# Performance work log

Hardware: AMD Instinct MI355X
Metric: run time of the kernel (lower is better)

Reference implementation:

```python
import jax, jax.numpy as jnp
import numpy as np

EPS = 1e-09


def _glorot(key, shape):
    fan_in, fan_out = shape[-2], shape[-1]
    std = (2.0 / (fan_in + fan_out)) ** 0.5
    return jax.random.normal(key, shape, dtype=jnp.float32) * std


def setup_inputs() -> dict:
    key = jax.random.key(0)
    kx, k1, k2, k3, k4 = jax.random.split(key, 5)
    B, S, D = 2, 1024, 256
    H, K = 8, 32  # key_dim_frac = 1/8
    return {
        "x": jax.random.normal(kx, (B, S, D), dtype=jnp.float32),
        "Wks": _glorot(k1, (H, D, K)),
        "Wqs": _glorot(k2, (H, D, K)),
        "Wvs": _glorot(k3, (H, D, D)),
        "Wo": _glorot(k4, (H, D, D)),
    }


def reference(x, Wks, Wqs, Wvs, Wo):
    # Per-head projections: [H, B, S, K] / [H, B, S, D]
    keys = jnp.einsum('bsd,hdk->hbsk', x, Wks)
    queries = jnp.einsum('bsd,hdk->hbsk', x, Wqs)
    values = jnp.einsum('bsd,hde->hbse', x, Wvs)

    # Feature map: elu + 1 (strictly positive)
    keys = jax.nn.elu(keys) + 1.0
    queries = jax.nn.elu(queries) + 1.0

    # Auxiliary pairwise attention map [H, B, S, S], causal-masked, row-normalized
    att = jnp.einsum('hbsk,hbtk->hbst', queries, keys)
    S = att.shape[-1]
    causal = jnp.tril(jnp.ones((S, S), dtype=att.dtype))
    att = att * causal
    att = att / (jnp.sum(att, axis=-1, keepdims=True) + EPS)

    # Causal linear attention via cumulative sums of outer products
    # [H, B, S, D, K] cumulative state (memory-bound, mirrors tf.cumsum)
    kv = jnp.einsum('hbsk,hbsd->hbsdk', keys, values)
    kv_cum = jnp.cumsum(kv, axis=2)
    numerator = jnp.einsum('hbsdk,hbsk->hbsd', kv_cum, queries)
    denominator = jnp.einsum('hbsk,hbsk->hbs', jnp.cumsum(keys, axis=2), queries)
    node = numerator / (denominator[..., None] + EPS)

    # Output projection, summed over heads: [B, S, D]
    out = jnp.einsum('hbsd,hde->bse', node, Wo)
    return (out, att)
```

## Files before the change

kernel.cpp:

```cpp
#include <hip/hip_runtime.h>
#include <hip/hip_bf16.h>
#include <cstdio>

#define PB 2
#define PS 1024
#define PD 256
#define PK 32
#define HB (PH*PB)
#define PH 8
#define BS (PB*PS)
#define EPS 1e-9f

typedef __attribute__((ext_vector_type(8))) short bf16x8;
typedef __attribute__((ext_vector_type(4))) float f32x4;

__device__ inline unsigned short f2bf(float f) {
    __hip_bfloat16 h = __float2bfloat16(f);
    return *reinterpret_cast<unsigned short*>(&h);
}

__global__ void k_xb(const float* __restrict__ x, unsigned short* __restrict__ xb) {
    int i = blockIdx.x*256 + threadIdx.x;
    float4 v = ((const float4*)x)[i];
    ushort4 o = {f2bf(v.x), f2bf(v.y), f2bf(v.z), f2bf(v.w)};
    ((ushort4*)xb)[i] = o;
}

__global__ void k_transpose_qk(const float* __restrict__ Wqs, const float* __restrict__ Wks,
                               unsigned short* __restrict__ WqT, unsigned short* __restrict__ WkT) {
    int h = blockIdx.x;
    const float* S = (blockIdx.y ? Wks : Wqs) + (size_t)h*8192;
    unsigned short* D = (blockIdx.y ? WkT : WqT) + (size_t)h*8192;
    __shared__ float T[256*33];
    int tid = threadIdx.x;
#pragma unroll
    for (int p = 0; p < 32; ++p) {
        int idx = p*256 + tid;
        T[(idx>>5)*33 + (idx&31)] = S[idx];
    }
    __syncthreads();
#pragma unroll
    for (int p = 0; p < 8; ++p) {
        int o4 = p*256 + tid;
        int kk = o4 >> 6, d = (o4 & 63)*4;
        ushort4 o;
        o.x = f2bf(T[(d+0)*33 + kk]); o.y = f2bf(T[(d+1)*33 + kk]);
        o.z = f2bf(T[(d+2)*33 + kk]); o.w = f2bf(T[(d+3)*33 + kk]);
        *(ushort4*)(D + (size_t)kk*256 + d) = o;
    }
}

__global__ void k_transpose256(const float* __restrict__ src, unsigned short* __restrict__ dst,
                               int dst_row_stride, int dst_head_stride) {
    int e0 = blockIdx.x*64, d0 = blockIdx.y*64, h = blockIdx.z;
    __shared__ float T[64][69];
    const float* S = src + (size_t)h*65536;
    int ty = threadIdx.x>>4, c4 = threadIdx.x&15;
#pragma unroll
    for (int p = 0; p < 4; ++p) {
        int r = p*16 + ty;
        float4 v = *(const float4*)(S + (size_t)(d0+r)*256 + e0 + c4*4);
        T[r][c4*4+0]=v.x; T[r][c4*4+1]=v.y; T[r][c4*4+2]=v.z; T[r][c4*4+3]=v.w;
    }
    __syncthreads();
    unsigned short* D = dst + (size_t)h*dst_head_stride;
#pragma unroll
    for (int p = 0; p < 4; ++p) {
        int er = p*16 + ty;
        ushort4 o;
        o.x = f2bf(T[c4*4+0][er]); o.y = f2bf(T[c4*4+1][er]);
        o.z = f2bf(T[c4*4+2][er]); o.w = f2bf(T[c4*4+3][er]);
        *(ushort4*)(D + (size_t)(e0+er)*dst_row_stride + d0 + c4*4) = o;
    }
}

__global__ __launch_bounds__(256) void k_proj_qk_mfma(
    const unsigned short* __restrict__ xb, const unsigned short* __restrict__ WqT,
    const unsigned short* __restrict__ WkT,
    float* __restrict__ Q, float* __restrict__ Kf,
    unsigned short* __restrict__ Qb, unsigned short* __restrict__ Kb)
{
    int m0 = blockIdx.x*64;
    int isK = blockIdx.y;
    int n0 = blockIdx.z*64;
    const unsigned short* W = isK ? WkT : WqT;
    int tid = threadIdx.x, w = tid>>6, l15 = tid&15, g = (tid>>4)&3;
    f32x4 zf = {0.f,0.f,0.f,0.f};
    f32x4 acc[4] = {zf,zf,zf,zf};
    const unsigned short* arow = xb + (size_t)(m0+16*w+l15)*256 + 8*g;
#pragma unroll
    for (int kk = 0; kk < 8; ++kk) {
        bf16x8 af = *(const bf16x8*)(arow + kk*32);
#pragma unroll
        for (int nt = 0; nt < 4; ++nt) {
            bf16x8 bf = *(const bf16x8*)(W + (size_t)(n0+16*nt+l15)*256 + kk*32 + 8*g);
            acc[nt] = __builtin_amdgcn_mfma_f32_16x16x32_bf16(af, bf, acc[nt], 0, 0, 0);
        }
    }
    int bs_base = m0 + 16*w + 4*g;
#pragma unroll
    for (int nt = 0; nt < 4; ++nt) {
        int col = n0 + 16*nt + l15;
        int h = col>>5, kk = col&31;
#pragma unroll
        for (int j = 0; j < 4; ++j) {
            int bs = bs_base + j;
            int b = bs>>10, s = bs&1023;
            float z = acc[nt][j];
            z = z > 0.f ? z + 1.f : expf(z);
            size_t idx = ((size_t)(h*PB+b)*PS + s)*PK + kk;
            if (isK) { Kf[idx] = z; Kb[idx] = f2bf(z); }
            else     { Q[idx]  = z; Qb[idx] = f2bf(z); }
        }
    }
}

__global__ void k_cumsum(const float* __restrict__ Kf, float* __restrict__ cumK) {
    int hb  = blockIdx.x;
    int tid = threadIdx.x;
    int c = tid >> 5, kk = tid & 31;
    const float* src = Kf   + hb*(PS*PK) + c*128*PK + kk;
    float*       dst = cumK + hb*(PS*PK) + c*128*PK + kk;
    float sum = 0.f;
#pragma unroll 8
    for (int i = 0; i < 128; ++i) sum += src[i*PK];
    __shared__ float ssum[8][32];
    ssum[c][kk] = sum;
    __syncthreads();
    float acc = 0.f;
    for (int j = 0; j < c; ++j) acc += ssum[j][kk];
#pragma unroll 8
    for (int i = 0; i < 128; ++i) { acc += src[i*PK]; dst[i*PK] = acc; }
}

__global__ void k_den(const float* __restrict__ Q, const float* __restrict__ cumK,
                      float* __restrict__ den) {
    int i = blockIdx.x*256 + threadIdx.x;
    const float4* q  = (const float4*)(Q    + (size_t)i*PK);
    const float4* ck = (const float4*)(cumK + (size_t)i*PK);
    float acc = 0.f;
#pragma unroll
    for (int j = 0; j < 8; ++j) {
        float4 a = q[j], b = ck[j];
        acc += a.x*b.x + a.y*b.y + a.z*b.z + a.w*b.w;
    }
    den[i] = acc + EPS;
}

__global__ __launch_bounds__(256) void k_proj_v_mfma(
    const unsigned short* __restrict__ xb, const unsigned short* __restrict__ WvT,
    unsigned short* __restrict__ Vt)
{
    int e0 = blockIdx.x*64, m0 = blockIdx.y*64, h = blockIdx.z;
    int tid = threadIdx.x, w = tid>>6, l15 = tid&15, g = (tid>>4)&3;
    f32x4 zf = {0.f,0.f,0.f,0.f};
    f32x4 acc[4] = {zf,zf,zf,zf};
    const unsigned short* arow = xb + (size_t)(m0+16*w+l15)*256 + 8*g;
    const unsigned short* Wb = WvT + (size_t)h*65536;
#pragma unroll
    for (int kk = 0; kk < 8; ++kk) {
        bf16x8 af = *(const bf16x8*)(arow + kk*32);
#pragma unroll
        for (int nt = 0; nt < 4; ++nt) {
            bf16x8 bf = *(const bf16x8*)(Wb + (size_t)(e0+16*nt+l15)*256 + kk*32 + 8*g);
            acc[nt] = __builtin_amdgcn_mfma_f32_16x16x32_bf16(af, bf, acc[nt], 0, 0, 0);
        }
    }
    unsigned short* VtT = Vt + ((size_t)h*32 + blockIdx.y)*(256*64);
#pragma unroll
    for (int nt = 0; nt < 4; ++nt) {
        ushort4 o = {f2bf(acc[nt][0]), f2bf(acc[nt][1]), f2bf(acc[nt][2]), f2bf(acc[nt][3])};
        *(ushort4*)(VtT + (size_t)(e0+16*nt+l15)*64 + 16*w + 4*g) = o;
    }
}

__global__ void k_att_zero(float* __restrict__ att) {
    int st = blockIdx.x;
    int hb = blockIdx.y;
    int s0 = st * 64;
    int c0 = s0 + 64;
    int nz4 = (PS - c0) >> 2;
    float* base = att + (size_t)hb*PS*PS + (size_t)s0*PS + c0;
    int r = threadIdx.x >> 2;
    int l4 = threadIdx.x & 3;
    float4 z = {0.f, 0.f, 0.f, 0.f};
    for (int c4 = l4; c4 < nz4; c4 += 4)
        *(float4*)(base + (size_t)r*PS + c4*4) = z;
}

__global__ __launch_bounds__(256) void k_fused(
    const unsigned short* __restrict__ Qb, const unsigned short* __restrict__ Kb,
    const float* __restrict__ den, const unsigned short* __restrict__ Vt,
    float* __restrict__ att, unsigned short* __restrict__ nodeB)
{
    int yy = blockIdx.x;
    int st = (yy & 1) ? (15 - (yy >> 1)) : (yy >> 1);
    int hb = blockIdx.y;
    int s0 = st * 64;
    int tid = threadIdx.x;
    int w = tid >> 6, l15 = tid & 15, g = (tid >> 4) & 3;

    __shared__ unsigned short VtL[256*72];
    __shared__ unsigned short PL[64*72];
    __shared__ float rden[64];

    bf16x8 qf = *(const bf16x8*)(Qb + ((size_t)hb*PS + s0 + 16*w + l15)*PK + 8*g);
    if (tid < 64) rden[tid] = 1.0f / den[hb*PS + s0 + tid];

    f32x4 zf = {0.f, 0.f, 0.f, 0.f};
    f32x4 acc2[4][4];
#pragma unroll
    for (int i = 0; i < 4; ++i)
#pragma unroll
        for (int j = 0; j < 4; ++j) acc2[i][j] = zf;

    float* attb = att + (size_t)hb*PS*PS;

    for (int t0 = 0; t0 <= s0; t0 += 64) {
        __syncthreads();
        const float4* src = (const float4*)(Vt + ((size_t)hb*16 + (t0 >> 6))*(256*64));
#pragma unroll
        for (int rep = 0; rep < 8; ++rep) {
            int idx = tid + rep*256;
            float4 v = src[idx];
            int e = idx >> 3, q = idx & 7;
            *(float4*)(VtL + e*72 + q*8) = v;
        }
        f32x4 p[4];
#pragma unroll
        for (int nt = 0; nt < 4; ++nt) {
            bf16x8 kf = *(const bf16x8*)(Kb + ((size_t)hb*PS + t0 + 16*nt + l15)*PK + 8*g);
            p[nt] = __builtin_amdgcn_mfma_f32_16x16x32_bf16(qf, kf, zf, 0, 0, 0);
        }
        bool diag = (t0 == s0);
        int rb = 16*w + 4*g;
#pragma unroll
        for (int nt = 0; nt < 4; ++nt) {
#pragma unroll
            for (int j = 0; j < 4; ++j) {
                int r = rb + j;
                int t = t0 + 16*nt + l15;
                float v = p[nt][j] * rden[r];
                if (diag && t > s0 + r) v = 0.f;
                attb[(size_t)(s0 + r)*PS + t] = v;
                PL[r*72 + 16*nt + l15] = f2bf(v);
            }
        }
        __syncthreads();
#pragma unroll
        for (int c = 0; c < 2; ++c) {
            bf16x8 af[4];
#pragma unroll
            for (int mt = 0; mt < 4; ++mt)
                af[mt] = *(const bf16x8*)(PL + (16*mt + l15)*72 + 32*c + 8*g);
#pragma unroll
            for (int ntl = 0; ntl < 4; ++ntl) {
                bf16x8 vf = *(const bf16x8*)(VtL + (16*(4*w + ntl) + l15)*72 + 32*c + 8*g);
#pragma unroll
                for (int mt = 0; mt < 4; ++mt)
                    acc2[mt][ntl] = __builtin_amdgcn_mfma_f32_16x16x32_bf16(af[mt], vf, acc2[mt][ntl], 0, 0, 0);
            }
        }
    }
    int h = hb >> 1, b = hb & 1;
    unsigned short* np = nodeB + ((size_t)(b*PS + s0))*2048 + h*256;
#pragma unroll
    for (int mt = 0; mt < 4; ++mt)
#pragma unroll
        for (int ntl = 0; ntl < 4; ++ntl)
#pragma unroll
            for (int j = 0; j < 4; ++j)
                np[(size_t)(16*mt + 4*g + j)*2048 + 64*w + 16*ntl + l15] = f2bf(acc2[mt][ntl][j]);
}

__global__ __launch_bounds__(256) void k_out_mfma(
    const unsigned short* __restrict__ nodeB, const unsigned short* __restrict__ WoT,
    float* __restrict__ part)
{
    int e0 = blockIdx.x*64, m0 = blockIdx.y*64, kz = blockIdx.z;
    int tid = threadIdx.x, w = tid>>6, l15 = tid&15, g = (tid>>4)&3;
    f32x4 zf = {0.f,0.f,0.f,0.f};
    f32x4 acc[4] = {zf,zf,zf,zf};
    const unsigned short* arow = nodeB + (size_t)(m0+16*w+l15)*2048 + kz*1024 + 8*g;
    const unsigned short* brow = WoT + kz*1024 + 8*g;
#pragma unroll
    for (int kk = 0; kk < 32; ++kk) {
        bf16x8 af = *(const bf16x8*)(arow + kk*32);
#pragma unroll
        for (int nt = 0; nt < 4; ++nt) {
            bf16x8 bf = *(const bf16x8*)(brow + (size_t)(e0+16*nt+l15)*2048 + kk*32);
            acc[nt] = __builtin_amdgcn_mfma_f32_16x16x32_bf16(af, bf, acc[nt], 0, 0, 0);
        }
    }
    float* P = part + (size_t)kz*BS*PD;
#pragma unroll
    for (int nt = 0; nt < 4; ++nt)
#pragma unroll
        for (int j = 0; j < 4; ++j)
            P[(size_t)(m0+16*w+4*g+j)*PD + e0+16*nt+l15] = acc[nt][j];
}

__global__ void k_reduce2(const float* __restrict__ part, float* __restrict__ out) {
    int i = blockIdx.x*256 + threadIdx.x;
    const float4* p = (const float4*)part;
    float4 a = p[i], b = p[131072 + i];
    float4 o = {a.x+b.x, a.y+b.y, a.z+b.z, a.w+b.w};
    ((float4*)out)[i] = o;
}

extern "C" void kernel_launch(void* const* d_in, const int* in_sizes, int n_in,
                              void* d_out, int out_size, void* d_ws, size_t ws_size,
                              hipStream_t stream) {
    const float* x   = (const float*)d_in[0];
    const float* Wks = (const float*)d_in[1];
    const float* Wqs = (const float*)d_in[2];
    const float* Wvs = (const float*)d_in[3];
    const float* Wo  = (const float*)d_in[4];

    float* out = (float*)d_out;
    float* att = (float*)d_out + (size_t)PB*PS*PD;

    float* ws = (float*)d_ws;
    float*          Q     = ws + 0;
    float*          Kf    = ws + 524288;
    float*          cumK  = ws + 1048576;
    float*          den   = ws + 1572864;
    unsigned short* Qb    = (unsigned short*)(ws + 1589248);
    unsigned short* Kb    = (unsigned short*)(ws + 1851392);
    unsigned short* Vt    = (unsigned short*)(ws + 2113536);
    unsigned short* xb    = (unsigned short*)(ws + 4210688);
    unsigned short* WqT   = (unsigned short*)(ws + 4472832);
    unsigned short* WkT   = (unsigned short*)(ws + 4505600);
    unsigned short* WvT   = (unsigned short*)(ws + 4538368);
    unsigned short* WoT   = (unsigned short*)(ws + 4800512);
    unsigned short* nodeB = (unsigned short*)(ws + 5062656);
    float*          part  = ws + 7159808;
    const size_t needed = (size_t)8208384 * 4;
    if (ws_size < needed) {
        fprintf(stderr, "kernel_launch: ws_size %zu < needed %zu\n", ws_size, needed);
        return;
    }

    k_xb<<<512, 256, 0, stream>>>(x, xb);
    k_transpose_qk<<<dim3(PH, 2), 256, 0, stream>>>(Wqs, Wks, WqT, WkT);
    k_transpose256<<<dim3(4, 4, PH), 256, 0, stream>>>(Wvs, WvT, 256, 65536);
    k_transpose256<<<dim3(4, 4, PH), 256, 0, stream>>>(Wo,  WoT, 2048, 256);
    k_proj_qk_mfma<<<dim3(32, 2, 4), 256, 0, stream>>>(xb, WqT, WkT, Q, Kf, Qb, Kb);
    k_cumsum<<<HB, 256, 0, stream>>>(Kf, cumK);
    k_den<<<64, 256, 0, stream>>>(Q, cumK, den);
    k_proj_v_mfma<<<dim3(4, 32, PH), 256, 0, stream>>>(xb, WvT, Vt);
    k_att_zero<<<dim3(15, HB), 256, 0, stream>>>(att);
    k_fused<<<dim3(16, HB), 256, 0, stream>>>(Qb, Kb, den, Vt, att, nodeB);
    k_out_mfma<<<dim3(4, 32, 2), 256, 0, stream>>>(nodeB, WoT, part);
    k_reduce2<<<512, 256, 0, stream>>>(part, out);
}
```

Baseline: 120.9 us.

## Replace quadratic causal attention-times-V with chunked KV prefix state

The node computation no longer walks all earlier 64-row tiles multiplying the normalized attention by V. Instead it builds per-chunk K^T V sums, scans them into bf16 exclusive prefix states, and computes each chunk as Q·KVprefix plus the intra-chunk diagonal block. Off-diagonal attention tiles are written by a separate fully parallel kernel. The output projection is rewritten to do the full K reduction in one kernel, which drops the partial-sum buffer and the reduce pass. The bf16 rounding of the prefix state adds some precision risk, and the change adds launches.

```diff
diff --git a/kernel.cpp b/kernel.cpp
--- a/kernel.cpp
+++ b/kernel.cpp
@@ -6,8 +6,8 @@
 #define PS 1024
 #define PD 256
 #define PK 32
+#define PH 8
 #define HB (PH*PB)
-#define PH 8
 #define BS (PB*PS)
 #define EPS 1e-9f
 
@@ -188,124 +188,172 @@
         *(float4*)(base + (size_t)r*PS + c4*4) = z;
 }
 
-__global__ __launch_bounds__(256) void k_fused(
+__global__ __launch_bounds__(256) void k_att_low(
+    const unsigned short* __restrict__ Qb, const unsigned short* __restrict__ Kb,
+    const float* __restrict__ den, float* __restrict__ att)
+{
+    int tt = blockIdx.x, st = blockIdx.y, hb = blockIdx.z;
+    if (tt >= st) return;
+    int s0 = st*64, t0 = tt*64;
+    int tid = threadIdx.x, w = tid>>6, l15 = tid&15, g = (tid>>4)&3;
+    f32x4 zf = {0.f,0.f,0.f,0.f};
+    bf16x8 qf = *(const bf16x8*)(Qb + ((size_t)hb*PS + s0 + 16*w + l15)*PK + 8*g);
+    f32x4 p[4];
+#pragma unroll
+    for (int nt = 0; nt < 4; ++nt) {
+        bf16x8 kf = *(const bf16x8*)(Kb + ((size_t)hb*PS + t0 + 16*nt + l15)*PK + 8*g);
+        p[nt] = __builtin_amdgcn_mfma_f32_16x16x32_bf16(qf, kf, zf, 0, 0, 0);
+    }
+    float* attb = att + (size_t)hb*PS*PS;
+    float rd[4];
+#pragma unroll
+    for (int j = 0; j < 4; ++j) rd[j] = 1.0f / den[hb*PS + s0 + 16*w + 4*g + j];
+#pragma unroll
+    for (int nt = 0; nt < 4; ++nt)
+#pragma unroll
+        for (int j = 0; j < 4; ++j)
+            attb[(size_t)(s0 + 16*w + 4*g + j)*PS + t0 + 16*nt + l15] = p[nt][j] * rd[j];
+}
+
+__global__ __launch_bounds__(256) void k_kv_sums(
+    const unsigned short* __restrict__ Kb, const unsigned short* __restrict__ Vt,
+    float* __restrict__ KVs)
+{
+    int c = blockIdx.x, hb = blockIdx.y;
+    int tid = threadIdx.x, w = tid>>6, l15 = tid&15, g = (tid>>4)&3;
+    __shared__ unsigned short KT[32*72];
+#pragma unroll
+    for (int i = 0; i < 8; ++i) {
+        int flat = tid + i*256;
+        KT[(flat&31)*72 + (flat>>5)] = Kb[((size_t)hb*PS + c*64 + (flat>>5))*PK + (flat&31)];
+    }
+    __syncthreads();
+    const unsigned short* Vtt = Vt + ((size_t)hb*16 + c)*(256*64);
+    f32x4 zf = {0.f,0.f,0.f,0.f};
+    f32x4 acc[4][2];
+#pragma unroll
+    for (int mt = 0; mt < 4; ++mt) { acc[mt][0] = zf; acc[mt][1] = zf; }
+#pragma unroll
+    for (int ks = 0; ks < 2; ++ks) {
+        bf16x8 af[4];
+#pragma unroll
+        for (int mt = 0; mt < 4; ++mt)
+            af[mt] = *(const bf16x8*)(Vtt + (size_t)(64*w + 16*mt + l15)*64 + 32*ks + 8*g);
+#pragma unroll
+        for (int nt = 0; nt < 2; ++nt) {
+            bf16x8 bf = *(const bf16x8*)(KT + (16*nt + l15)*72 + 32*ks + 8*g);
+#pragma unroll
+            for (int mt = 0; mt < 4; ++mt)
+                acc[mt][nt] = __builtin_amdgcn_mfma_f32_16x16x32_bf16(af[mt], bf, acc[mt][nt], 0, 0, 0);
+        }
+    }
+    float* o = KVs + ((size_t)hb*16 + c)*8192;
+#pragma unroll
+    for (int mt = 0; mt < 4; ++mt)
+#pragma unroll
+        for (int nt = 0; nt < 2; ++nt)
+#pragma unroll
+            for (int j = 0; j < 4; ++j)
+                o[(size_t)(64*w + 16*mt + 4*g + j)*32 + 16*nt + l15] = acc[mt][nt][j];
+}
+
+__global__ void k_kv_scan(const float* __restrict__ KVs, unsigned short* __restrict__ KVpre) {
+    int hb = blockIdx.y;
+    int i = blockIdx.x*256 + threadIdx.x;
+    const float* src = KVs + (size_t)hb*16*8192 + i;
+    unsigned short* dst = KVpre + (size_t)hb*16*8192 + i;
+    float acc = 0.f;
+#pragma unroll
+    for (int c = 0; c < 16; ++c) { dst[c*8192] = f2bf(acc); acc += src[c*8192]; }
+}
+
+__global__ __launch_bounds__(256) void k_node(
     const unsigned short* __restrict__ Qb, const unsigned short* __restrict__ Kb,
     const float* __restrict__ den, const unsigned short* __restrict__ Vt,
+    const unsigned short* __restrict__ KVpre,
     float* __restrict__ att, unsigned short* __restrict__ nodeB)
 {
-    int yy = blockIdx.x;
-    int st = (yy & 1) ? (15 - (yy >> 1)) : (yy >> 1);
-    int hb = blockIdx.y;
-    int s0 = st * 64;
-    int tid = threadIdx.x;
-    int w = tid >> 6, l15 = tid & 15, g = (tid >> 4) & 3;
-
-    __shared__ unsigned short VtL[256*72];
+    int c = blockIdx.x, hb = blockIdx.y;
+    int s0 = c*64;
+    int tid = threadIdx.x, w = tid>>6, l15 = tid&15, g = (tid>>4)&3;
     __shared__ unsigned short PL[64*72];
     __shared__ float rden[64];
-
+    if (tid < 64) rden[tid] = 1.0f / den[hb*PS + s0 + tid];
+
+    f32x4 zf = {0.f,0.f,0.f,0.f};
     bf16x8 qf = *(const bf16x8*)(Qb + ((size_t)hb*PS + s0 + 16*w + l15)*PK + 8*g);
-    if (tid < 64) rden[tid] = 1.0f / den[hb*PS + s0 + tid];
-
-    f32x4 zf = {0.f, 0.f, 0.f, 0.f};
-    f32x4 acc2[4][4];
-#pragma unroll
-    for (int i = 0; i < 4; ++i)
-#pragma unroll
-        for (int j = 0; j < 4; ++j) acc2[i][j] = zf;
-
+
+    const unsigned short* KVp = KVpre + ((size_t)hb*16 + c)*8192;
+    f32x4 acc[16];
+#pragma unroll
+    for (int nt = 0; nt < 16; ++nt) {
+        bf16x8 bf = *(const bf16x8*)(KVp + (size_t)(16*nt + l15)*32 + 8*g);
+        acc[nt] = __builtin_amdgcn_mfma_f32_16x16x32_bf16(qf, bf, zf, 0, 0, 0);
+    }
+    f32x4 p[4];
+#pragma unroll
+    for (int nt4 = 0; nt4 < 4; ++nt4) {
+        bf16x8 kf = *(const bf16x8*)(Kb + ((size_t)hb*PS + s0 + 16*nt4 + l15)*PK + 8*g);
+        p[nt4] = __builtin_amdgcn_mfma_f32_16x16x32_bf16(qf, kf, zf, 0, 0, 0);
+    }
+    __syncthreads();
     float* attb = att + (size_t)hb*PS*PS;
-
-    for (int t0 = 0; t0 <= s0; t0 += 64) {
-        __syncthreads();
-        const float4* src = (const float4*)(Vt + ((size_t)hb*16 + (t0 >> 6))*(256*64));
-#pragma unroll
-        for (int rep = 0; rep < 8; ++rep) {
-            int idx = tid + rep*256;
-            float4 v = src[idx];
-            int e = idx >> 3, q = idx & 7;
-            *(float4*)(VtL + e*72 + q*8) = v;
-        }
-        f32x4 p[4];
-#pragma unroll
-        for (int nt = 0; nt < 4; ++nt) {
-            bf16x8 kf = *(const bf16x8*)(Kb + ((size_t)hb*PS + t0 + 16*nt + l15)*PK + 8*g);
-            p[nt] = __builtin_amdgcn_mfma_f32_16x16x32_bf16(qf, kf, zf, 0, 0, 0);
-        }
-        bool diag = (t0 == s0);
-        int rb = 16*w + 4*g;
-#pragma unroll
-        for (int nt = 0; nt < 4; ++nt) {
-#pragma unroll
-            for (int j = 0; j < 4; ++j) {
-                int r = rb + j;
-                int t = t0 + 16*nt + l15;
-                float v = p[nt][j] * rden[r];
-                if (diag && t > s0 + r) v = 0.f;
-                attb[(size_t)(s0 + r)*PS + t] = v;
-                PL[r*72 + 16*nt + l15] = f2bf(v);
-            }
-        }
-        __syncthreads();
-#pragma unroll
-        for (int c = 0; c < 2; ++c) {
-            bf16x8 af[4];
-#pragma unroll
-            for (int mt = 0; mt < 4; ++mt)
-                af[mt] = *(const bf16x8*)(PL + (16*mt + l15)*72 + 32*c + 8*g);
-#pragma unroll
-            for (int ntl = 0; ntl < 4; ++ntl) {
-                bf16x8 vf = *(const bf16x8*)(VtL + (16*(4*w + ntl) + l15)*72 + 32*c + 8*g);
-#pragma unroll
-                for (int mt = 0; mt < 4; ++mt)
-                    acc2[mt][ntl] = __builtin_amdgcn_mfma_f32_16x16x32_bf16(af[mt], vf, acc2[mt][ntl], 0, 0, 0);
-            }
+#pragma unroll
+    for (int nt4 = 0; nt4 < 4; ++nt4) {
+#pragma unroll
+        for (int j = 0; j < 4; ++j) {
+            int r = 16*w + 4*g + j;
+            int tc = 16*nt4 + l15;
+            float v = p[nt4][j] * rden[r];
+            if (tc > r) v = 0.f;
+            attb[(size_t)(s0 + r)*PS + s0 + tc] = v;
+            PL[r*72 + tc] = f2bf(v);
+        }
+    }
+#pragma unroll
+    for (int nt = 0; nt < 16; ++nt)
+#pragma unroll
+        for (int j = 0; j < 4; ++j)
+            acc[nt][j] *= rden[16*w + 4*g + j];
+    __syncthreads();
+    const unsigned short* Vtt = Vt + ((size_t)hb*16 + c)*(256*64);
+#pragma unroll
+    for (int ks = 0; ks < 2; ++ks) {
+        bf16x8 af = *(const bf16x8*)(PL + (size_t)(16*w + l15)*72 + 32*ks + 8*g);
+#pragma unroll
+        for (int nt = 0; nt < 16; ++nt) {
+            bf16x8 vf = *(const bf16x8*)(Vtt + (size_t)(16*nt + l15)*64 + 32*ks + 8*g);
+            acc[nt] = __builtin_amdgcn_mfma_f32_16x16x32_bf16(af, vf, acc[nt], 0, 0, 0);
         }
     }
     int h = hb >> 1, b = hb & 1;
     unsigned short* np = nodeB + ((size_t)(b*PS + s0))*2048 + h*256;
 #pragma unroll
-    for (int mt = 0; mt < 4; ++mt)
-#pragma unroll
-        for (int ntl = 0; ntl < 4; ++ntl)
-#pragma unroll
-            for (int j = 0; j < 4; ++j)
-                np[(size_t)(16*mt + 4*g + j)*2048 + 64*w + 16*ntl + l15] = f2bf(acc2[mt][ntl][j]);
-}
-
-__global__ __launch_bounds__(256) void k_out_mfma(
+    for (int nt = 0; nt < 16; ++nt)
+#pragma unroll
+        for (int j = 0; j < 4; ++j)
+            np[(size_t)(16*w + 4*g + j)*2048 + 16*nt + l15] = f2bf(acc[nt][j]);
+}
+
+__global__ __launch_bounds__(256) void k_out2(
     const unsigned short* __restrict__ nodeB, const unsigned short* __restrict__ WoT,
-    float* __restrict__ part)
-{
-    int e0 = blockIdx.x*64, m0 = blockIdx.y*64, kz = blockIdx.z;
-    int tid = threadIdx.x, w = tid>>6, l15 = tid&15, g = (tid>>4)&3;
-    f32x4 zf = {0.f,0.f,0.f,0.f};
-    f32x4 acc[4] = {zf,zf,zf,zf};
-    const unsigned short* arow = nodeB + (size_t)(m0+16*w+l15)*2048 + kz*1024 + 8*g;
-    const unsigned short* brow = WoT + kz*1024 + 8*g;
-#pragma unroll
-    for (int kk = 0; kk < 32; ++kk) {
+    float* __restrict__ out)
+{
+    int e0 = blockIdx.x*64, m0 = blockIdx.y*16;
+    int tid = threadIdx.x, w = tid>>6, l15 = tid&15, g = (tid>>4)&3;
+    f32x4 zf = {0.f,0.f,0.f,0.f};
+    f32x4 acc = zf;
+    const unsigned short* arow = nodeB + (size_t)(m0 + l15)*2048 + 8*g;
+    const unsigned short* brow = WoT + (size_t)(e0 + 16*w + l15)*2048 + 8*g;
+#pragma unroll 8
+    for (int kk = 0; kk < 64; ++kk) {
         bf16x8 af = *(const bf16x8*)(arow + kk*32);
-#pragma unroll
-        for (int nt = 0; nt < 4; ++nt) {
-            bf16x8 bf = *(const bf16x8*)(brow + (size_t)(e0+16*nt+l15)*2048 + kk*32);
-            acc[nt] = __builtin_amdgcn_mfma_f32_16x16x32_bf16(af, bf, acc[nt], 0, 0, 0);
-        }
-    }
-    float* P = part + (size_t)kz*BS*PD;
-#pragma unroll
-    for (int nt = 0; nt < 4; ++nt)
-#pragma unroll
-        for (int j = 0; j < 4; ++j)
-            P[(size_t)(m0+16*w+4*g+j)*PD + e0+16*nt+l15] = acc[nt][j];
-}
-
-__global__ void k_reduce2(const float* __restrict__ part, float* __restrict__ out) {
-    int i = blockIdx.x*256 + threadIdx.x;
-    const float4* p = (const float4*)part;
-    float4 a = p[i], b = p[131072 + i];
-    float4 o = {a.x+b.x, a.y+b.y, a.z+b.z, a.w+b.w};
-    ((float4*)out)[i] = o;
+        bf16x8 bf = *(const bf16x8*)(brow + kk*32);
+        acc = __builtin_amdgcn_mfma_f32_16x16x32_bf16(af, bf, acc, 0, 0, 0);
+    }
+#pragma unroll
+    for (int j = 0; j < 4; ++j)
+        out[(size_t)(m0 + 4*g + j)*PD + e0 + 16*w + l15] = acc[j];
 }
 
 extern "C" void kernel_launch(void* const* d_in, const int* in_sizes, int n_in,
@@ -324,18 +372,19 @@
     float*          Q     = ws + 0;
     float*          Kf    = ws + 524288;
     float*          cumK  = ws + 1048576;
-    float*          den   = ws + 1572864;
-    unsigned short* Qb    = (unsigned short*)(ws + 1589248);
-    unsigned short* Kb    = (unsigned short*)(ws + 1851392);
-    unsigned short* Vt    = (unsigned short*)(ws + 2113536);
-    unsigned short* xb    = (unsigned short*)(ws + 4210688);
-    unsigned short* WqT   = (unsigned short*)(ws + 4472832);
-    unsigned short* WkT   = (unsigned short*)(ws + 4505600);
-    unsigned short* WvT   = (unsigned short*)(ws + 4538368);
-    unsigned short* WoT   = (unsigned short*)(ws + 4800512);
-    unsigned short* nodeB = (unsigned short*)(ws + 5062656);
-    float*          part  = ws + 7159808;
-    const size_t needed = (size_t)8208384 * 4;
+    float*          KVs   = ws + 0;
+    float*          den   = ws + 2097152;
+    unsigned short* Qb    = (unsigned short*)(ws + 2113536);
+    unsigned short* Kb    = (unsigned short*)(ws + 2375680);
+    unsigned short* Vt    = (unsigned short*)(ws + 2637824);
+    unsigned short* xb    = (unsigned short*)(ws + 4734976);
+    unsigned short* WqT   = (unsigned short*)(ws + 4997120);
+    unsigned short* WkT   = (unsigned short*)(ws + 5029888);
+    unsigned short* WvT   = (unsigned short*)(ws + 5062656);
+    unsigned short* WoT   = (unsigned short*)(ws + 5324800);
+    unsigned short* nodeB = (unsigned short*)(ws + 5586944);
+    unsigned short* KVpre = (unsigned short*)(ws + 7684096);
+    const size_t needed = (size_t)8732672 * 4;
     if (ws_size < needed) {
         fprintf(stderr, "kernel_launch: ws_size %zu < needed %zu\n", ws_size, needed);
         return;
@@ -350,7 +399,9 @@
     k_den<<<64, 256, 0, stream>>>(Q, cumK, den);
     k_proj_v_mfma<<<dim3(4, 32, PH), 256, 0, stream>>>(xb, WvT, Vt);
     k_att_zero<<<dim3(15, HB), 256, 0, stream>>>(att);
-    k_fused<<<dim3(16, HB), 256, 0, stream>>>(Qb, Kb, den, Vt, att, nodeB);
-    k_out_mfma<<<dim3(4, 32, 2), 256, 0, stream>>>(nodeB, WoT, part);
-    k_reduce2<<<512, 256, 0, stream>>>(part, out);
-}
+    k_att_low<<<dim3(16, 16, HB), 256, 0, stream>>>(Qb, Kb, den, att);
+    k_kv_sums<<<dim3(16, HB), 256, 0, stream>>>(Kb, Vt, KVs);
+    k_kv_scan<<<dim3(32, HB), 256, 0, stream>>>(KVs, KVpre);
+    k_node<<<dim3(16, HB), 256, 0, stream>>>(Qb, Kb, den, Vt, KVpre, att, nodeB);
+    k_out2<<<dim3(4, 128), 256, 0, stream>>>(nodeB, WoT, out);
+}
```

Result: slower. 126.3 us (+4.5%).
